# Performance work log

Hardware: AMD Instinct MI355X
Metric: run time of the kernel (lower is better)

The kernel has to match this reference:

```python
import jax, jax.numpy as jnp
import numpy as np
from math import sqrt

EPS = 1e-5
N_BISECT = 30

def _entmax15_impl(x):
    # alpha=1.5 entmax along last axis via bisection (entmax_bisect, alpha=1.5)
    xs = x * 0.5  # (alpha-1) * x
    mx = jnp.max(xs, axis=-1, keepdims=True)
    d = xs.shape[-1]
    lo = mx - 1.0
    hi = mx - d ** -0.5  # d^{-(alpha-1)}
    def body(i, carry):
        lo, hi = carry
        mid = 0.5 * (lo + hi)
        f = jnp.sum(jnp.square(jnp.maximum(xs - mid, 0.0)), -1, keepdims=True) - 1.0
        lo = jnp.where(f > 0, mid, lo)
        hi = jnp.where(f > 0, hi, mid)
        return lo, hi
    lo, hi = jax.lax.fori_loop(0, N_BISECT, body, (lo, hi))
    tau = 0.5 * (lo + hi)
    p = jnp.square(jnp.maximum(xs - tau, 0.0))
    return p / jnp.sum(p, -1, keepdims=True)

@jax.custom_vjp
def entmax15(x):
    return _entmax15_impl(x)

def _entmax15_fwd(x):
    p = _entmax15_impl(x)
    return p, p

def _entmax15_bwd(p, g):
    # exact entmax-1.5 backward (entmax repo): gppr = sqrt(p) on support
    s = jnp.sqrt(p)
    dx = g * s
    q = jnp.sum(dx, -1, keepdims=True) / jnp.sum(s, -1, keepdims=True)
    return (dx - q * s,)

entmax15.defvjp(_entmax15_fwd, _entmax15_bwd)

def layer_norm(x, g, b):
    m = jnp.mean(x, -1, keepdims=True)
    v = jnp.var(x, -1, keepdims=True)
    return (x - m) / jnp.sqrt(v + EPS) * g + b

def mlp(x, w1, b1, w2, b2):
    return jax.nn.gelu(x @ w1 + b1, approximate=False) @ w2 + b2

def hopfield_core(q_in, k_in, H, wq, bq, wk, bk, wv, bv, wo, bo):
    # Faithful to Hopfield.forward with mix=True; `values` arg of the torch
    # module is ignored (it recomputes value_projection(key_projection(keys))).
    B, L, _ = q_in.shape
    S = k_in.shape[1]
    q = (q_in @ wq + bq).reshape(B, L, H, -1)
    k = k_in @ wk + bk
    v = (k @ wv + bv).reshape(B, S, H, -1)
    kh = k.reshape(B, S, H, -1)
    E = q.shape[-1]
    scores = jnp.einsum('blhe,bshe->bhls', q, kh) * (1.0 / sqrt(E))
    A = entmax15(scores)
    out = jnp.einsum('bhls,bshd->blhd', A, v)
    # mix=True: transpose(2,1) then view(B, L, -1) on contiguous (B,H,L,D)
    out = jnp.transpose(out, (0, 2, 1, 3)).reshape(B, L, -1)
    return out @ wo + bo

def _forward(n_heads, x, ct_wq, ct_bq, ct_wk, ct_bk, ct_wv, ct_bv, ct_wo, ct_bo,
             cs_wq, cs_bq, cs_wk, cs_bk, cs_wv, cs_bv, cs_wo, cs_bo, cs_key,
             hp_wq, hp_bq, hp_wk, hp_bk, hp_wv, hp_bv, hp_wo, hp_bo,
             n1_g, n1_b, n2_g, n2_b, n3_g, n3_b, n4_g, n4_b,
             m1_w1, m1_b1, m1_w2, m1_b2, m2_w1, m2_b1, m2_w2, m2_b2):
    b, ts_d, seg, d = x.shape
    time_in = x.reshape(b * ts_d, seg, d)
    time_enc = hopfield_core(time_in, time_in, n_heads,
                             ct_wq, ct_bq, ct_wk, ct_bk, ct_wv, ct_bv, ct_wo, ct_bo)
    dim_in = layer_norm(time_in + time_enc, n1_g, n1_b)
    dim_in = layer_norm(dim_in + mlp(dim_in, m1_w1, m1_b1, m1_w2, m1_b2), n2_g, n2_b)
    # '(b ts_d) seg d -> (b seg) ts_d d'
    series_in = dim_in.reshape(b, ts_d, seg, d).transpose(0, 2, 1, 3).reshape(b * seg, ts_d, d)
    # HopfieldPooling: learned stored patterns as keys
    pooled_keys = jnp.broadcast_to(cs_key, (b * seg,) + cs_key.shape[1:])
    series_h = hopfield_core(series_in, pooled_keys, n_heads,
                             cs_wq, cs_bq, cs_wk, cs_bk, cs_wv, cs_bv, cs_wo, cs_bo)
    pooled_h = hopfield_core(series_in, series_in, n_heads,
                             hp_wq, hp_bq, hp_wk, hp_bk, hp_wv, hp_bv, hp_wo, hp_bo)
    dim_enc = layer_norm(series_h + pooled_h, n3_g, n3_b)
    dim_enc = layer_norm(dim_enc + mlp(dim_enc, m2_w1, m2_b1, m2_w2, m2_b2), n4_g, n4_b)
    # '(b seg) ts_d d -> b ts_d seg d'
    return dim_enc.reshape(b, seg, ts_d, d).transpose(0, 2, 1, 3)

def setup_inputs() -> dict:
    b, ts_d, seg, d, h, dff, factor = 8, 32, 64, 1024, 16, 4096, 10
    keys = iter(jax.random.split(jax.random.key(0), 64))
    def rn(shape, s=0.02):
        return jax.random.normal(next(keys), shape, jnp.float32) * s
    inp = {"x": jax.random.normal(next(keys), (b, ts_d, seg, d), jnp.float32)}
    for p in ("ct", "cs", "hp"):
        inp[p + "_wq"] = rn((d, d)); inp[p + "_bq"] = rn((d,))
        inp[p + "_wk"] = rn((d, d)); inp[p + "_bk"] = rn((d,))
        inp[p + "_wv"] = rn((d, d)); inp[p + "_bv"] = rn((d,))
        inp[p + "_wo"] = rn((d, d)); inp[p + "_bo"] = rn((d,))
    inp["cs_key"] = rn((1, factor, d), 0.1)
    for i in ("1", "2", "3", "4"):
        inp["n" + i + "_g"] = jnp.ones((d,), jnp.float32)
        inp["n" + i + "_b"] = jnp.zeros((d,), jnp.float32)
    for m in ("m1", "m2"):
        inp[m + "_w1"] = rn((d, dff)); inp[m + "_b1"] = rn((dff,))
        inp[m + "_w2"] = rn((dff, d)); inp[m + "_b2"] = rn((d,))
    inp["n_heads"] = h
    return inp

def reference(x, ct_wq, ct_bq, ct_wk, ct_bk, ct_wv, ct_bv, ct_wo, ct_bo,
              cs_wq, cs_bq, cs_wk, cs_bk, cs_wv, cs_bv, cs_wo, cs_bo, cs_key,
              hp_wq, hp_bq, hp_wk, hp_bk, hp_wv, hp_bv, hp_wo, hp_bo,
              n1_g, n1_b, n2_g, n2_b, n3_g, n3_b, n4_g, n4_b,
              m1_w1, m1_b1, m1_w2, m1_b2, m2_w1, m2_b1, m2_w2, m2_b2, n_heads):
    return _forward(n_heads, x, ct_wq, ct_bq, ct_wk, ct_bk, ct_wv, ct_bv, ct_wo, ct_bo,
                    cs_wq, cs_bq, cs_wk, cs_bk, cs_wv, cs_bv, cs_wo, cs_bo, cs_key,
                    hp_wq, hp_bq, hp_wk, hp_bk, hp_wv, hp_bv, hp_wo, hp_bo,
                    n1_g, n1_b, n2_g, n2_b, n3_g, n3_b, n4_g, n4_b,
                    m1_w1, m1_b1, m1_w2, m1_b2, m2_w1, m2_b1, m2_w2, m2_b2)
```

## Files before the change

### kernel.cpp

```cpp
#include <hip/hip_runtime.h>
#include <cstdio>

typedef __bf16 bf16x8 __attribute__((ext_vector_type(8)));
typedef float f32x4 __attribute__((ext_vector_type(4)));
typedef int i32x4 __attribute__((ext_vector_type(4)));
typedef unsigned short u16x4 __attribute__((ext_vector_type(4)));

__device__ __forceinline__ float bf2f(unsigned short u) {
  union { unsigned int i; float f; } x; x.i = ((unsigned int)u) << 16; return x.f;
}
__device__ __forceinline__ unsigned short f2bf(float f) {
  union { float f; unsigned int i; } x; x.f = f;
  unsigned int r = x.i + 0x7fffu + ((x.i >> 16) & 1u);
  return (unsigned short)(r >> 16);
}

__device__ __forceinline__ void gl2lds16(const unsigned short* g, unsigned short* l) {
  __builtin_amdgcn_global_load_lds((const __attribute__((address_space(1))) unsigned int*)g,
                                   (__attribute__((address_space(3))) unsigned int*)l, 16, 0, 0);
}

__global__ __launch_bounds__(256) void k_cast(const float* __restrict__ in,
                                              unsigned short* __restrict__ out, int n4) {
  int i = blockIdx.x * 256 + threadIdx.x;
  if (i >= n4) return;
  f32x4 v = ((const f32x4*)in)[i];
  u16x4 o;
  o[0] = f2bf(v[0]); o[1] = f2bf(v[1]); o[2] = f2bf(v[2]); o[3] = f2bf(v[3]);
  ((u16x4*)out)[i] = o;
}

__global__ __launch_bounds__(256) void k_tcast(const float* __restrict__ src,
                                               unsigned short* __restrict__ dst,
                                               int K, int N) {
  __shared__ float tile[32][33];
  int gx = blockIdx.x * 32;
  int gy = blockIdx.y * 32;
  int t = threadIdx.x;
  int c = t & 31, r0 = t >> 5;
#pragma unroll
  for (int i = 0; i < 4; i++) {
    int r = r0 + i * 8;
    tile[r][c] = src[(size_t)(gy + r) * N + gx + c];
  }
  __syncthreads();
#pragma unroll
  for (int i = 0; i < 4; i++) {
    int r = r0 + i * 8;
    dst[(size_t)(gx + r) * K + gy + c] = f2bf(tile[c][r]);
  }
}

__global__ __launch_bounds__(256) void k_bfold(const float* __restrict__ bk,
                                               const float* __restrict__ wv,
                                               const float* __restrict__ bv,
                                               float* __restrict__ out) {
  int n = blockIdx.x * 256 + threadIdx.x;
  float acc = bv[n];
#pragma unroll 8
  for (int j = 0; j < 1024; j++) acc += bk[j] * wv[(size_t)j * 1024 + n];
  out[n] = acc;
}

__global__ __launch_bounds__(256) void k_cpb(const float* __restrict__ a,
                                             const float* __restrict__ b,
                                             float* __restrict__ out) {
  int t = blockIdx.x * 256 + threadIdx.x;
  out[t] = a[t];
  out[1024 + t] = b[t];
}

template <bool GELU>
__global__ __launch_bounds__(256) void k_gemm(const unsigned short* __restrict__ A,
                                              const unsigned short* __restrict__ Bt,
                                              const float* __restrict__ bias,
                                              unsigned short* __restrict__ C,
                                              int M, int N, int K) {
  __shared__ unsigned short As[3][128 * 32];
  __shared__ unsigned short Bs[3][128 * 32];
  const int rowA0 = blockIdx.y * 128, colB0 = blockIdx.x * 128;
  const int t = threadIdx.x, w = t >> 6, lane = t & 63;
  const int wr = w >> 1, wc = w & 1;
  const int srow = w * 16 + (lane >> 2);
  const int schunk = (lane & 3) ^ ((lane >> 3) & 3);
  const unsigned short* pa = A + (size_t)(rowA0 + srow) * K + schunk * 8;
  const unsigned short* pb = Bt + (size_t)(colB0 + srow) * K + schunk * 8;
  const size_t row64 = (size_t)64 * K;

  f32x4 acc[4][4] = {};
  const int g = lane >> 4, ra = lane & 15;
  const int gp8 = (g ^ ((ra >> 1) & 3)) * 8;

  auto stage = [&](int buf, int kk) {
    gl2lds16(pa + kk,         &As[buf][w * 512]);
    gl2lds16(pa + row64 + kk, &As[buf][2048 + w * 512]);
    gl2lds16(pb + kk,         &Bs[buf][w * 512]);
    gl2lds16(pb + row64 + kk, &Bs[buf][2048 + w * 512]);
  };

  const int NT = K >> 5;
  stage(0, 0);
  if (NT > 1) stage(1, 32);
  int cur = 0;
  for (int j = 0; j < NT; ++j) {
    if (j + 1 < NT) asm volatile("s_waitcnt vmcnt(4)" ::: "memory");
    else            asm volatile("s_waitcnt vmcnt(0)" ::: "memory");
    __builtin_amdgcn_sched_barrier(0);
    __builtin_amdgcn_s_barrier();
    __builtin_amdgcn_sched_barrier(0);
    if (j + 2 < NT) {
      int nb = cur + 2; if (nb >= 3) nb -= 3;
      stage(nb, (j + 2) * 32);
    }
    bf16x8 af[4], bfr[4];
#pragma unroll
    for (int m = 0; m < 4; m++)
      af[m] = *(const bf16x8*)&As[cur][(wr * 64 + m * 16 + ra) * 32 + gp8];
#pragma unroll
    for (int n = 0; n < 4; n++)
      bfr[n] = *(const bf16x8*)&Bs[cur][(wc * 64 + n * 16 + ra) * 32 + gp8];
#pragma unroll
    for (int m = 0; m < 4; m++)
#pragma unroll
      for (int n = 0; n < 4; n++)
        acc[m][n] = __builtin_amdgcn_mfma_f32_16x16x32_bf16(af[m], bfr[n], acc[m][n], 0, 0, 0);
    cur += 1; if (cur >= 3) cur -= 3;
  }
  asm volatile("s_waitcnt vmcnt(0) lgkmcnt(0)" ::: "memory");
  __builtin_amdgcn_s_barrier();

  unsigned short* Ep = &As[0][0] + w * 1024;
  const int grow0 = rowA0 + wr * 64;
  const int gcol0 = colB0 + wc * 64;
  float bv[4];
#pragma unroll
  for (int n = 0; n < 4; n++) bv[n] = bias ? bias[gcol0 + n * 16 + ra] : 0.f;
  const int rdrow = lane >> 3, rg = lane & 7;
#pragma unroll
  for (int m = 0; m < 4; m++) {
#pragma unroll
    for (int n = 0; n < 4; n++)
#pragma unroll
      for (int i = 0; i < 4; i++) {
        int r = g * 4 + i;
        float v = acc[m][n][i] + bv[n];
        if (GELU) v = 0.5f * v * (1.f + erff(v * 0.70710678118654752f));
        Ep[r * 64 + ((ra + n * 16) ^ ((r & 7) << 3))] = f2bf(v);
      }
    asm volatile("s_waitcnt lgkmcnt(0)" ::: "memory");
    __builtin_amdgcn_sched_barrier(0);
#pragma unroll
    for (int p = 0; p < 2; p++) {
      int rr = p * 8 + rdrow;
      bf16x8 val = *(const bf16x8*)&Ep[rr * 64 + ((rg ^ (rr & 7)) << 3)];
      *(bf16x8*)&C[(size_t)(grow0 + m * 16 + rr) * N + gcol0 + rg * 8] = val;
    }
    asm volatile("s_waitcnt lgkmcnt(0)" ::: "memory");
  }
}

__global__ __launch_bounds__(256) void k_gemm10(const unsigned short* __restrict__ A,
                                                const unsigned short* __restrict__ Bt,
                                                const float* __restrict__ bias,
                                                unsigned short* __restrict__ C) {
  __shared__ float af[1024];
  int m = blockIdx.x, nb = blockIdx.y;
  int t = threadIdx.x;
#pragma unroll
  for (int i = 0; i < 4; i++) af[t * 4 + i] = bf2f(A[(size_t)m * 1024 + t * 4 + i]);
  __syncthreads();
  int w = t >> 6, lane = t & 63;
  for (int n = nb * 64 + w; n < nb * 64 + 64; n += 4) {
    const unsigned short* brow = Bt + (size_t)n * 1024 + lane * 16;
    float acc = 0.f;
#pragma unroll
    for (int j = 0; j < 16; j++) acc += af[lane * 16 + j] * bf2f(brow[j]);
#pragma unroll
    for (int o = 32; o; o >>= 1) acc += __shfl_xor(acc, o);
    if (lane == 0) C[(size_t)m * 1024 + n] = f2bf(acc + bias[n]);
  }
}

template <int L, int S, bool SHARED>
__global__ __launch_bounds__(256) void k_attn(const unsigned short* __restrict__ Q,
                                              const unsigned short* __restrict__ Kb,
                                              const unsigned short* __restrict__ Vb,
                                              unsigned short* __restrict__ Out, int RS) {
  constexpr int SP = (S <= 32) ? 32 : 64;
  constexpr int QST = 72;
  constexpr int VST = SP + 8;
  constexpr int CST = SP + 4;
  __shared__ unsigned short Qs[L * QST];
  __shared__ unsigned short Ks[SP * QST];
  __shared__ unsigned short Vt[64 * VST];
  __shared__ float Sc[L * CST];
  __shared__ float Rps[L];
  const int blk = blockIdx.x, batch = blk >> 4, h = blk & 15;
  const int t = threadIdx.x, w = t >> 6, lane = t & 63;

  for (int c = t; c < L * 8; c += 256) {
    int r = c >> 3, ch = (c & 7) * 8;
    *(i32x4*)&Qs[r * QST + ch] =
        *(const i32x4*)&Q[((size_t)(batch * L + r)) * RS + h * 64 + ch];
  }
  for (int c = t; c < SP * 8; c += 256) {
    int r = c >> 3, ch = (c & 7) * 8;
    i32x4 v = {0, 0, 0, 0};
    if (r < S) {
      size_t rb = SHARED ? (size_t)r : (size_t)(batch * S + r);
      v = *(const i32x4*)&Kb[rb * RS + h * 64 + ch];
    }
    *(i32x4*)&Ks[r * QST + ch] = v;
  }
  for (int c = t; c < SP * 64; c += 256) {
    int s = c >> 6, e = c & 63;
    unsigned short v = 0;
    if (s < S) {
      size_t rb = SHARED ? (size_t)s : (size_t)(batch * S + s);
      v = Vb[rb * RS + h * 64 + e];
    }
    Vt[e * VST + s] = v;
  }
  __syncthreads();

  const int ka = (lane >> 4) * 8, ra = lane & 15;
  const int cr = (lane >> 4) * 4, cc = lane & 15;
  constexpr int NT = SP / 16, TT = (L / 16) * NT;
  for (int tt = w; tt < TT; tt += 4) {
    int m = tt / NT, n = tt % NT;
    f32x4 a = {0.f, 0.f, 0.f, 0.f};
#pragma unroll
    for (int ks = 0; ks < 2; ks++) {
      bf16x8 af = *(const bf16x8*)&Qs[(m * 16 + ra) * QST + ks * 32 + ka];
      bf16x8 bf = *(const bf16x8*)&Ks[(n * 16 + ra) * QST + ks * 32 + ka];
      a = __builtin_amdgcn_mfma_f32_16x16x32_bf16(af, bf, a, 0, 0, 0);
    }
#pragma unroll
    for (int i = 0; i < 4; i++)
      Sc[(m * 16 + cr + i) * CST + n * 16 + cc] = a[i] * 0.0625f;
  }
  __syncthreads();

  constexpr int G = 256 / L, RW = 64 / G, SL = SP / G;
  const int row = w * RW + lane / G, sub = lane % G;
  float xs[SL];
#pragma unroll
  for (int j = 0; j < SL; j++) {
    int s = sub * SL + j;
    float v = Sc[row * CST + s];
    if (S < SP && s >= S) v = -1e30f;
    xs[j] = v;
  }
  float mx = xs[0];
#pragma unroll
  for (int j = 1; j < SL; j++) mx = fmaxf(mx, xs[j]);
#pragma unroll
  for (int o = G / 2; o; o >>= 1) mx = fmaxf(mx, __shfl_xor(mx, o));
  const float hoff = (S == 64) ? 0.125f : (S == 32) ? 0.17677669529663687f : 0.31622776601683794f;
  float lo = mx - 1.f, hi = mx - hoff;
#pragma unroll 1
  for (int it = 0; it < 26; it++) {
    float mid = 0.5f * (lo + hi);
    float f = 0.f;
#pragma unroll
    for (int j = 0; j < SL; j++) { float dd = fmaxf(xs[j] - mid, 0.f); f += dd * dd; }
#pragma unroll
    for (int o = G / 2; o; o >>= 1) f += __shfl_xor(f, o);
    bool gt = f > 1.f;
    lo = gt ? mid : lo;
    hi = gt ? hi : mid;
  }
  float tau = 0.5f * (lo + hi);
  float ps = 0.f;
#pragma unroll
  for (int j = 0; j < SL; j++) { float dd = fmaxf(xs[j] - tau, 0.f); xs[j] = dd * dd; ps += xs[j]; }
#pragma unroll
  for (int o = G / 2; o; o >>= 1) ps += __shfl_xor(ps, o);
  if (sub == 0) Rps[row] = 1.f / ps;
  unsigned short* Pb = Qs;
#pragma unroll
  for (int j = 0; j < SL; j += 4) {
    u16x4 pv;
#pragma unroll
    for (int jj = 0; jj < 4; jj++) pv[jj] = f2bf(xs[j + jj]);
    *(u16x4*)&Pb[row * VST + sub * SL + j] = pv;
  }
  __syncthreads();

  constexpr int TT2 = (L / 16) * 4;
  for (int tt = w; tt < TT2; tt += 4) {
    int m = tt >> 2, n = tt & 3;
    f32x4 a = {0.f, 0.f, 0.f, 0.f};
#pragma unroll
    for (int ks = 0; ks < SP / 32; ks++) {
      bf16x8 af = *(const bf16x8*)&Pb[(m * 16 + ra) * VST + ks * 32 + ka];
      bf16x8 bf = *(const bf16x8*)&Vt[(n * 16 + ra) * VST + ks * 32 + ka];
      a = __builtin_amdgcn_mfma_f32_16x16x32_bf16(af, bf, a, 0, 0, 0);
    }
#pragma unroll
    for (int i = 0; i < 4; i++) {
      int l = m * 16 + cr + i, e = n * 16 + cc;
      float val = a[i] * Rps[l];
      int l_new = h * (L / 16) + (l >> 4);
      int cg = (l & 15) * 64 + e;
      Out[((size_t)(batch * L + l_new)) * 1024 + cg] = f2bf(val);
    }
  }
}

template <int MODE, bool F32OUT>
__global__ __launch_bounds__(256) void k_ln(const unsigned short* __restrict__ a,
                                            const unsigned short* __restrict__ b,
                                            const float* __restrict__ g,
                                            const float* __restrict__ be,
                                            void* __restrict__ outp) {
  __shared__ float red[8];
  int r = blockIdx.x, t = threadIdx.x;
  size_t base = (size_t)r * 1024 + t * 4;
  u16x4 av = *(const u16x4*)(a + base);
  u16x4 bv = *(const u16x4*)(b + base);
  float x[4];
  float s = 0.f, ss = 0.f;
#pragma unroll
  for (int i = 0; i < 4; i++) {
    x[i] = bf2f(av[i]) + bf2f(bv[i]);
    s += x[i]; ss += x[i] * x[i];
  }
#pragma unroll
  for (int o = 32; o; o >>= 1) { s += __shfl_xor(s, o); ss += __shfl_xor(ss, o); }
  int w = t >> 6;
  if ((t & 63) == 0) { red[w] = s; red[4 + w] = ss; }
  __syncthreads();
  s = red[0] + red[1] + red[2] + red[3];
  ss = red[4] + red[5] + red[6] + red[7];
  float mean = s * (1.f / 1024.f);
  float var = ss * (1.f / 1024.f) - mean * mean;
  float rstd = rsqrtf(var + 1e-5f);
  int orow;
  if (MODE == 0) orow = r;
  else if (MODE == 1) { int bi = r >> 11, rem = r & 2047; int tt = rem >> 6, sd = rem & 63; orow = (bi << 11) + sd * 32 + tt; }
  else { int bi = r >> 11, rem = r & 2047; int sd = rem >> 5, tt = rem & 31; orow = (bi << 11) + tt * 64 + sd; }
  size_t ob = (size_t)orow * 1024 + t * 4;
  if (F32OUT) {
    f32x4 y;
#pragma unroll
    for (int i = 0; i < 4; i++) y[i] = (x[i] - mean) * rstd * g[t * 4 + i] + be[t * 4 + i];
    *(f32x4*)((float*)outp + ob) = y;
  } else {
    u16x4 y;
#pragma unroll
    for (int i = 0; i < 4; i++) y[i] = f2bf((x[i] - mean) * rstd * g[t * 4 + i] + be[t * 4 + i]);
    *(u16x4*)((unsigned short*)outp + ob) = y;
  }
}


extern "C" void kernel_launch(void* const* d_in, const int* in_sizes, int n_in,
                              void* d_out, int out_size, void* d_ws, size_t ws_size,
                              hipStream_t stream) {
  const int M = 16384;
  if (n_in < 43 || in_sizes[0] != 16777216 || in_sizes[25] != 10240 || in_sizes[34] != 4194304) {
    fprintf(stderr, "kernel_launch: unexpected input layout (n_in=%d)\n", n_in);
    return;
  }
  const float* x = (const float*)d_in[0];
  const float* w[3][4]; const float* bia[3][4];
  for (int p = 0; p < 3; p++) {
    w[p][0] = (const float*)d_in[1 + 8 * p + 0]; bia[p][0] = (const float*)d_in[1 + 8 * p + 1];
    w[p][1] = (const float*)d_in[1 + 8 * p + 2]; bia[p][1] = (const float*)d_in[1 + 8 * p + 3];
    w[p][2] = (const float*)d_in[1 + 8 * p + 4]; bia[p][2] = (const float*)d_in[1 + 8 * p + 5];
    w[p][3] = (const float*)d_in[1 + 8 * p + 6]; bia[p][3] = (const float*)d_in[1 + 8 * p + 7];
  }
  const float* cs_key = (const float*)d_in[25];
  const float* ng[4]; const float* nb[4];
  for (int i = 0; i < 4; i++) { ng[i] = (const float*)d_in[26 + 2 * i]; nb[i] = (const float*)d_in[27 + 2 * i]; }
  const float* m_w1[2]; const float* m_b1[2]; const float* m_w2[2]; const float* m_b2[2];
  for (int i = 0; i < 2; i++) {
    m_w1[i] = (const float*)d_in[34 + 4 * i]; m_b1[i] = (const float*)d_in[35 + 4 * i];
    m_w2[i] = (const float*)d_in[36 + 4 * i]; m_b2[i] = (const float*)d_in[37 + 4 * i];
  }

  char* base = (char*)d_ws; size_t off = 0;
  auto alloc = [&](size_t bytes) -> void* {
    off = (off + 255) & ~(size_t)255;
    void* p = base + off; off += bytes; return p;
  };
  const size_t W1M = (size_t)1024 * 1024;
  unsigned short* W3ct = (unsigned short*)alloc(3 * W1M * 2);
  unsigned short* W3hp = (unsigned short*)alloc(3 * W1M * 2);
  unsigned short* Woct = (unsigned short*)alloc(W1M * 2);
  unsigned short* Wohp = (unsigned short*)alloc(W1M * 2);
  unsigned short* Wocs = (unsigned short*)alloc(W1M * 2);
  unsigned short* Wqcs = (unsigned short*)alloc(W1M * 2);
  unsigned short* Wkcs = (unsigned short*)alloc(W1M * 2);
  unsigned short* Wvcs = (unsigned short*)alloc(W1M * 2);
  unsigned short* Wm1u = (unsigned short*)alloc((size_t)4096 * 1024 * 2);
  unsigned short* Wm1d = (unsigned short*)alloc((size_t)1024 * 4096 * 2);
  unsigned short* Wm2u = (unsigned short*)alloc((size_t)4096 * 1024 * 2);
  unsigned short* Wm2d = (unsigned short*)alloc((size_t)1024 * 4096 * 2);
  unsigned short* Wvt_ct = (unsigned short*)alloc(W1M * 2);
  unsigned short* Wraw_ct = (unsigned short*)alloc(W1M * 2);
  unsigned short* Wvt_hp = (unsigned short*)alloc(W1M * 2);
  unsigned short* Wraw_hp = (unsigned short*)alloc(W1M * 2);
  float* b3ct = (float*)alloc(3072 * 4);
  float* b3hp = (float*)alloc(3072 * 4);
  unsigned short* P[5];
  for (int i = 0; i < 5; i++) P[i] = (unsigned short*)alloc((size_t)M * 1024 * 2);
  unsigned short* KeyB = (unsigned short*)alloc((size_t)10 * 1024 * 2);
  unsigned short* Kcs = (unsigned short*)alloc((size_t)10 * 1024 * 2);
  unsigned short* Vcs = (unsigned short*)alloc((size_t)10 * 1024 * 2);
  if (off > ws_size) {
    fprintf(stderr, "kernel_launch: ws too small: need %zu have %zu\n", off, ws_size);
    return;
  }
  const int MC = 8192;

  auto gemm = [&](const unsigned short* Ap, const unsigned short* Bt, const float* bi,
                  unsigned short* Cp, int Mm, int Nn, int Kk, bool gelu) {
    dim3 gg(Nn / 128, Mm / 128);
    if (gelu) k_gemm<true><<<gg, 256, 0, stream>>>(Ap, Bt, bi, Cp, Mm, Nn, Kk);
    else      k_gemm<false><<<gg, 256, 0, stream>>>(Ap, Bt, bi, Cp, Mm, Nn, Kk);
  };
  auto tc = [&](const float* src, unsigned short* dst) {
    k_tcast<<<dim3(32, 32), 256, 0, stream>>>(src, dst, 1024, 1024);
  };

  tc(w[0][0], W3ct); tc(w[0][1], W3ct + W1M);
  tc(w[2][0], W3hp); tc(w[2][1], W3hp + W1M);
  tc(w[0][3], Woct); tc(w[2][3], Wohp); tc(w[1][3], Wocs);
  tc(w[1][0], Wqcs); tc(w[1][1], Wkcs); tc(w[1][2], Wvcs);
  k_tcast<<<dim3(128, 32), 256, 0, stream>>>(m_w1[0], Wm1u, 1024, 4096);
  k_tcast<<<dim3(32, 128), 256, 0, stream>>>(m_w2[0], Wm1d, 4096, 1024);
  k_tcast<<<dim3(128, 32), 256, 0, stream>>>(m_w1[1], Wm2u, 1024, 4096);
  k_tcast<<<dim3(32, 128), 256, 0, stream>>>(m_w2[1], Wm2d, 4096, 1024);
  tc(w[0][2], Wvt_ct); k_cast<<<1024, 256, 0, stream>>>(w[0][1], Wraw_ct, 262144);
  tc(w[2][2], Wvt_hp); k_cast<<<1024, 256, 0, stream>>>(w[2][1], Wraw_hp, 262144);
  k_cast<<<16384, 256, 0, stream>>>(x, P[0], 16777216 / 4);
  k_cast<<<10, 256, 0, stream>>>(cs_key, KeyB, 10240 / 4);
  gemm(Wvt_ct, Wraw_ct, nullptr, W3ct + 2 * W1M, 1024, 1024, 1024, false);
  gemm(Wvt_hp, Wraw_hp, nullptr, W3hp + 2 * W1M, 1024, 1024, 1024, false);
  k_cpb<<<4, 256, 0, stream>>>(bia[0][0], bia[0][1], b3ct);
  k_bfold<<<4, 256, 0, stream>>>(bia[0][1], w[0][2], bia[0][2], b3ct + 2048);
  k_cpb<<<4, 256, 0, stream>>>(bia[2][0], bia[2][1], b3hp);
  k_bfold<<<4, 256, 0, stream>>>(bia[2][1], w[2][2], bia[2][2], b3hp + 2048);
  k_gemm10<<<dim3(10, 16), 256, 0, stream>>>(KeyB, Wkcs, bia[1][1], Kcs);
  k_gemm10<<<dim3(10, 16), 256, 0, stream>>>(Kcs, Wvcs, bia[1][2], Vcs);

  gemm(P[0], W3ct, b3ct, P[1], M, 3072, 1024, false);
  k_attn<64, 64, false><<<256 * 16, 256, 0, stream>>>(P[1], P[1] + 1024, P[1] + 2048, P[4], 3072);
  gemm(P[4], Woct, bia[0][3], P[1], M, 1024, 1024, false);
  k_ln<0, false><<<M, 256, 0, stream>>>(P[0], P[1], ng[0], nb[0], P[2]);
  for (int c = 0; c < M; c += MC) {
    gemm(P[2] + (size_t)c * 1024, Wm1u, m_b1[0], P[3], MC, 4096, 1024, true);
    gemm(P[3], Wm1d, m_b2[0], P[1] + (size_t)c * 1024, MC, 1024, 4096, false);
  }
  k_ln<1, false><<<M, 256, 0, stream>>>(P[2], P[1], ng[1], nb[1], P[3]);

  gemm(P[3], W3hp, b3hp, P[0], M, 3072, 1024, false);
  k_attn<32, 32, false><<<512 * 16, 256, 0, stream>>>(P[0], P[0] + 1024, P[0] + 2048, P[4], 3072);
  gemm(P[4], Wohp, bia[2][3], P[1], M, 1024, 1024, false);
  gemm(P[3], Wqcs, bia[1][0], P[2], M, 1024, 1024, false);
  k_attn<32, 10, true><<<512 * 16, 256, 0, stream>>>(P[2], Kcs, Vcs, P[0], 1024);
  gemm(P[0], Wocs, bia[1][3], P[2], M, 1024, 1024, false);
  k_ln<0, false><<<M, 256, 0, stream>>>(P[2], P[1], ng[2], nb[2], P[0]);
  for (int c = 0; c < M; c += MC) {
    gemm(P[0] + (size_t)c * 1024, Wm2u, m_b1[1], P[2], MC, 4096, 1024, true);
    gemm(P[2], Wm2d, m_b2[1], P[1] + (size_t)c * 1024, MC, 1024, 4096, false);
  }
  k_ln<2, true><<<M, 256, 0, stream>>>(P[0], P[1], ng[3], nb[3], d_out);
}
```

Baseline: 1.825 ms.

## Switch main GEMMs to 256x256-tile 8-wave kernel with interleaved staging

```diff
diff --git a/kernel.cpp b/kernel.cpp
--- a/kernel.cpp
+++ b/kernel.cpp
@@ -71,11 +71,162 @@
 }
 
 template <bool GELU>
-__global__ __launch_bounds__(256) void k_gemm(const unsigned short* __restrict__ A,
-                                              const unsigned short* __restrict__ Bt,
-                                              const float* __restrict__ bias,
-                                              unsigned short* __restrict__ C,
-                                              int M, int N, int K) {
+__global__ __launch_bounds__(512, 2) void k_gemm8(const unsigned short* __restrict__ A,
+                                                  const unsigned short* __restrict__ Bt,
+                                                  const float* __restrict__ bias,
+                                                  unsigned short* __restrict__ C,
+                                                  int M, int N, int K) {
+  __shared__ unsigned short As[2][256 * 64];
+  __shared__ unsigned short Bs[2][256 * 64];
+  const int rowA0 = blockIdx.y * 256, colB0 = blockIdx.x * 256;
+  const int t = threadIdx.x, w = t >> 6, lane = t & 63;
+  const int wm = w >> 2, wn = w & 3;
+  const int g = lane >> 4, ra = lane & 15;
+  const int koff0 = (((0 * 4 + g) ^ (ra & 7)) * 8);
+  const int koff1 = (((1 * 4 + g) ^ (ra & 7)) * 8);
+  const int srow = w * 8 + (lane >> 3);
+  const int schunk = ((lane & 7) ^ ((lane >> 3) & 7)) * 8;
+
+  f32x4 acc[8][4] = {};
+
+  auto stageA = [&](int buf, int kk) {
+#pragma unroll
+    for (int gq = 0; gq < 4; gq++)
+      gl2lds16(A + (size_t)(rowA0 + gq * 64 + srow) * K + kk + schunk,
+               &As[buf][gq * 4096 + w * 512]);
+  };
+  auto stageB = [&](int buf, int kk) {
+#pragma unroll
+    for (int gq = 0; gq < 4; gq++)
+      gl2lds16(Bt + (size_t)(colB0 + gq * 64 + srow) * K + kk + schunk,
+               &Bs[buf][gq * 4096 + w * 512]);
+  };
+
+  const int NT = K >> 6;
+  stageA(0, 0); stageB(0, 0);
+  asm volatile("s_waitcnt vmcnt(0)" ::: "memory");
+  __builtin_amdgcn_sched_barrier(0);
+  __builtin_amdgcn_s_barrier();
+
+  bf16x8 aH[4][2], bH[2][2][2];
+  const int arow0 = wm * 128, brow0 = wn * 64;
+  for (int j = 0; j < NT; ++j) {
+    const int buf = j & 1;
+    const unsigned short* Ab = &As[buf][0];
+    const unsigned short* Bb = &Bs[buf][0];
+#pragma unroll
+    for (int fr = 0; fr < 4; fr++) {
+      aH[fr][0] = *(const bf16x8*)&Ab[(arow0 + fr * 16 + ra) * 64 + koff0];
+      aH[fr][1] = *(const bf16x8*)&Ab[(arow0 + fr * 16 + ra) * 64 + koff1];
+    }
+#pragma unroll
+    for (int fc = 0; fc < 2; fc++) {
+      bH[0][fc][0] = *(const bf16x8*)&Bb[(brow0 + fc * 16 + ra) * 64 + koff0];
+      bH[0][fc][1] = *(const bf16x8*)&Bb[(brow0 + fc * 16 + ra) * 64 + koff1];
+    }
+    if (j + 1 < NT) stageA(buf ^ 1, (j + 1) << 6);
+    __builtin_amdgcn_sched_barrier(0);
+    __builtin_amdgcn_s_barrier();
+    __builtin_amdgcn_sched_barrier(0);
+    __builtin_amdgcn_s_setprio(1);
+#pragma unroll
+    for (int fr = 0; fr < 4; fr++)
+#pragma unroll
+      for (int fc = 0; fc < 2; fc++)
+#pragma unroll
+        for (int ks = 0; ks < 2; ks++)
+          acc[fr][fc] = __builtin_amdgcn_mfma_f32_16x16x32_bf16(aH[fr][ks], bH[0][fc][ks], acc[fr][fc], 0, 0, 0);
+    __builtin_amdgcn_s_setprio(0);
+    __builtin_amdgcn_sched_barrier(0);
+    __builtin_amdgcn_s_barrier();
+#pragma unroll
+    for (int fc = 0; fc < 2; fc++) {
+      bH[1][fc][0] = *(const bf16x8*)&Bb[(brow0 + 32 + fc * 16 + ra) * 64 + koff0];
+      bH[1][fc][1] = *(const bf16x8*)&Bb[(brow0 + 32 + fc * 16 + ra) * 64 + koff1];
+    }
+    if (j + 1 < NT) stageB(buf ^ 1, (j + 1) << 6);
+    __builtin_amdgcn_sched_barrier(0);
+    __builtin_amdgcn_s_barrier();
+    __builtin_amdgcn_sched_barrier(0);
+    __builtin_amdgcn_s_setprio(1);
+#pragma unroll
+    for (int fr = 0; fr < 4; fr++)
+#pragma unroll
+      for (int fc = 0; fc < 2; fc++)
+#pragma unroll
+        for (int ks = 0; ks < 2; ks++)
+          acc[fr][2 + fc] = __builtin_amdgcn_mfma_f32_16x16x32_bf16(aH[fr][ks], bH[1][fc][ks], acc[fr][2 + fc], 0, 0, 0);
+    __builtin_amdgcn_s_setprio(0);
+    __builtin_amdgcn_sched_barrier(0);
+    __builtin_amdgcn_s_barrier();
+#pragma unroll
+    for (int fr = 0; fr < 4; fr++) {
+      aH[fr][0] = *(const bf16x8*)&Ab[(arow0 + 64 + fr * 16 + ra) * 64 + koff0];
+      aH[fr][1] = *(const bf16x8*)&Ab[(arow0 + 64 + fr * 16 + ra) * 64 + koff1];
+    }
+    __builtin_amdgcn_sched_barrier(0);
+    __builtin_amdgcn_s_barrier();
+    __builtin_amdgcn_sched_barrier(0);
+    __builtin_amdgcn_s_setprio(1);
+#pragma unroll
+    for (int fr = 0; fr < 4; fr++)
+#pragma unroll
+      for (int fc = 0; fc < 2; fc++)
+#pragma unroll
+        for (int ks = 0; ks < 2; ks++)
+          acc[4 + fr][fc] = __builtin_amdgcn_mfma_f32_16x16x32_bf16(aH[fr][ks], bH[0][fc][ks], acc[4 + fr][fc], 0, 0, 0);
+    __builtin_amdgcn_s_setprio(0);
+    __builtin_amdgcn_sched_barrier(0);
+    __builtin_amdgcn_s_barrier();
+    __builtin_amdgcn_s_setprio(1);
+#pragma unroll
+    for (int fr = 0; fr < 4; fr++)
+#pragma unroll
+      for (int fc = 0; fc < 2; fc++)
+#pragma unroll
+        for (int ks = 0; ks < 2; ks++)
+          acc[4 + fr][2 + fc] = __builtin_amdgcn_mfma_f32_16x16x32_bf16(aH[fr][ks], bH[1][fc][ks], acc[4 + fr][2 + fc], 0, 0, 0);
+    __builtin_amdgcn_s_setprio(0);
+    if (j + 1 < NT) asm volatile("s_waitcnt vmcnt(0)" ::: "memory");
+    __builtin_amdgcn_sched_barrier(0);
+    __builtin_amdgcn_s_barrier();
+  }
+
+  unsigned short* Ep = &As[0][0] + w * 1024;
+  const int grow0 = rowA0 + wm * 128;
+  const int gcol0 = colB0 + wn * 64;
+  float bv[4];
+#pragma unroll
+  for (int n = 0; n < 4; n++) bv[n] = bias ? bias[gcol0 + n * 16 + ra] : 0.f;
+  const int rdrow = lane >> 3, rg = lane & 7;
+#pragma unroll
+  for (int m = 0; m < 8; m++) {
+#pragma unroll
+    for (int n = 0; n < 4; n++)
+#pragma unroll
+      for (int i = 0; i < 4; i++) {
+        int r = g * 4 + i;
+        float v = acc[m][n][i] + bv[n];
+        if (GELU) v = 0.5f * v * (1.f + erff(v * 0.70710678118654752f));
+        Ep[r * 64 + ((ra + n * 16) ^ ((r & 7) << 3))] = f2bf(v);
+      }
+    asm volatile("s_waitcnt lgkmcnt(0)" ::: "memory");
+    __builtin_amdgcn_sched_barrier(0);
+#pragma unroll
+    for (int p = 0; p < 2; p++) {
+      int rr = p * 8 + rdrow;
+      bf16x8 val = *(const bf16x8*)&Ep[rr * 64 + ((rg ^ (rr & 7)) << 3)];
+      *(bf16x8*)&C[(size_t)(grow0 + m * 16 + rr) * N + gcol0 + rg * 8] = val;
+    }
+    asm volatile("s_waitcnt lgkmcnt(0)" ::: "memory");
+  }
+}
+
+__global__ __launch_bounds__(256) void k_gemmS(const unsigned short* __restrict__ A,
+                                               const unsigned short* __restrict__ Bt,
+                                               const float* __restrict__ bias,
+                                               unsigned short* __restrict__ C,
+                                               int M, int N, int K) {
   __shared__ unsigned short As[3][128 * 32];
   __shared__ unsigned short Bs[3][128 * 32];
   const int rowA0 = blockIdx.y * 128, colB0 = blockIdx.x * 128;
@@ -86,18 +237,15 @@
   const unsigned short* pa = A + (size_t)(rowA0 + srow) * K + schunk * 8;
   const unsigned short* pb = Bt + (size_t)(colB0 + srow) * K + schunk * 8;
   const size_t row64 = (size_t)64 * K;
-
   f32x4 acc[4][4] = {};
   const int g = lane >> 4, ra = lane & 15;
   const int gp8 = (g ^ ((ra >> 1) & 3)) * 8;
-
   auto stage = [&](int buf, int kk) {
-    gl2lds16(pa + kk,         &As[buf][w * 512]);
+    gl2lds16(pa + kk, &As[buf][w * 512]);
     gl2lds16(pa + row64 + kk, &As[buf][2048 + w * 512]);
-    gl2lds16(pb + kk,         &Bs[buf][w * 512]);
+    gl2lds16(pb + kk, &Bs[buf][w * 512]);
     gl2lds16(pb + row64 + kk, &Bs[buf][2048 + w * 512]);
   };
-
   const int NT = K >> 5;
   stage(0, 0);
   if (NT > 1) stage(1, 32);
@@ -105,13 +253,8 @@
   for (int j = 0; j < NT; ++j) {
     if (j + 1 < NT) asm volatile("s_waitcnt vmcnt(4)" ::: "memory");
     else            asm volatile("s_waitcnt vmcnt(0)" ::: "memory");
-    __builtin_amdgcn_sched_barrier(0);
-    __builtin_amdgcn_s_barrier();
-    __builtin_amdgcn_sched_barrier(0);
-    if (j + 2 < NT) {
-      int nb = cur + 2; if (nb >= 3) nb -= 3;
-      stage(nb, (j + 2) * 32);
-    }
+    __syncthreads();
+    if (j + 2 < NT) { int nb = cur + 2; if (nb >= 3) nb -= 3; stage(nb, (j + 2) * 32); }
     bf16x8 af[4], bfr[4];
 #pragma unroll
     for (int m = 0; m < 4; m++)
@@ -124,38 +267,21 @@
 #pragma unroll
       for (int n = 0; n < 4; n++)
         acc[m][n] = __builtin_amdgcn_mfma_f32_16x16x32_bf16(af[m], bfr[n], acc[m][n], 0, 0, 0);
+    __syncthreads();
     cur += 1; if (cur >= 3) cur -= 3;
   }
-  asm volatile("s_waitcnt vmcnt(0) lgkmcnt(0)" ::: "memory");
-  __builtin_amdgcn_s_barrier();
-
-  unsigned short* Ep = &As[0][0] + w * 1024;
-  const int grow0 = rowA0 + wr * 64;
-  const int gcol0 = colB0 + wc * 64;
-  float bv[4];
-#pragma unroll
-  for (int n = 0; n < 4; n++) bv[n] = bias ? bias[gcol0 + n * 16 + ra] : 0.f;
-  const int rdrow = lane >> 3, rg = lane & 7;
+  const int cr = g * 4, cc = ra;
 #pragma unroll
   for (int m = 0; m < 4; m++) {
-#pragma unroll
-    for (int n = 0; n < 4; n++)
-#pragma unroll
-      for (int i = 0; i < 4; i++) {
-        int r = g * 4 + i;
-        float v = acc[m][n][i] + bv[n];
-        if (GELU) v = 0.5f * v * (1.f + erff(v * 0.70710678118654752f));
-        Ep[r * 64 + ((ra + n * 16) ^ ((r & 7) << 3))] = f2bf(v);
-      }
-    asm volatile("s_waitcnt lgkmcnt(0)" ::: "memory");
-    __builtin_amdgcn_sched_barrier(0);
-#pragma unroll
-    for (int p = 0; p < 2; p++) {
-      int rr = p * 8 + rdrow;
-      bf16x8 val = *(const bf16x8*)&Ep[rr * 64 + ((rg ^ (rr & 7)) << 3)];
-      *(bf16x8*)&C[(size_t)(grow0 + m * 16 + rr) * N + gcol0 + rg * 8] = val;
-    }
-    asm volatile("s_waitcnt lgkmcnt(0)" ::: "memory");
+    int grow = rowA0 + wr * 64 + m * 16 + cr;
+#pragma unroll
+    for (int n = 0; n < 4; n++) {
+      int gcol = colB0 + wc * 64 + n * 16 + cc;
+      float bvv = bias ? bias[gcol] : 0.f;
+#pragma unroll
+      for (int i = 0; i < 4; i++)
+        C[(size_t)(grow + i) * N + gcol] = f2bf(acc[m][n][i] + bvv);
+    }
   }
 }
 
@@ -197,7 +323,6 @@
   __shared__ float Rps[L];
   const int blk = blockIdx.x, batch = blk >> 4, h = blk & 15;
   const int t = threadIdx.x, w = t >> 6, lane = t & 63;
-
   for (int c = t; c < L * 8; c += 256) {
     int r = c >> 3, ch = (c & 7) * 8;
     *(i32x4*)&Qs[r * QST + ch] =
@@ -222,7 +347,6 @@
     Vt[e * VST + s] = v;
   }
   __syncthreads();
-
   const int ka = (lane >> 4) * 8, ra = lane & 15;
   const int cr = (lane >> 4) * 4, cc = lane & 15;
   constexpr int NT = SP / 16, TT = (L / 16) * NT;
@@ -240,7 +364,6 @@
       Sc[(m * 16 + cr + i) * CST + n * 16 + cc] = a[i] * 0.0625f;
   }
   __syncthreads();
-
   constexpr int G = 256 / L, RW = 64 / G, SL = SP / G;
   const int row = w * RW + lane / G, sub = lane % G;
   float xs[SL];
@@ -286,7 +409,6 @@
     *(u16x4*)&Pb[row * VST + sub * SL + j] = pv;
   }
   __syncthreads();
-
   constexpr int TT2 = (L / 16) * 4;
   for (int tt = w; tt < TT2; tt += 4) {
     int m = tt >> 2, n = tt & 3;
@@ -398,28 +520,27 @@
   unsigned short* Wm1d = (unsigned short*)alloc((size_t)1024 * 4096 * 2);
   unsigned short* Wm2u = (unsigned short*)alloc((size_t)4096 * 1024 * 2);
   unsigned short* Wm2d = (unsigned short*)alloc((size_t)1024 * 4096 * 2);
-  unsigned short* Wvt_ct = (unsigned short*)alloc(W1M * 2);
-  unsigned short* Wraw_ct = (unsigned short*)alloc(W1M * 2);
-  unsigned short* Wvt_hp = (unsigned short*)alloc(W1M * 2);
-  unsigned short* Wraw_hp = (unsigned short*)alloc(W1M * 2);
   float* b3ct = (float*)alloc(3072 * 4);
   float* b3hp = (float*)alloc(3072 * 4);
-  unsigned short* P[5];
-  for (int i = 0; i < 5; i++) P[i] = (unsigned short*)alloc((size_t)M * 1024 * 2);
   unsigned short* KeyB = (unsigned short*)alloc((size_t)10 * 1024 * 2);
   unsigned short* Kcs = (unsigned short*)alloc((size_t)10 * 1024 * 2);
   unsigned short* Vcs = (unsigned short*)alloc((size_t)10 * 1024 * 2);
+  unsigned short* S[6];
+  for (int i = 0; i < 6; i++) S[i] = (unsigned short*)alloc((size_t)M * 1024 * 2);
   if (off > ws_size) {
     fprintf(stderr, "kernel_launch: ws too small: need %zu have %zu\n", off, ws_size);
     return;
   }
-  const int MC = 8192;
+  unsigned short* Wvt_ct = S[1];
+  unsigned short* Wraw_ct = S[1] + W1M;
+  unsigned short* Wvt_hp = S[1] + 2 * W1M;
+  unsigned short* Wraw_hp = S[1] + 3 * W1M;
 
   auto gemm = [&](const unsigned short* Ap, const unsigned short* Bt, const float* bi,
                   unsigned short* Cp, int Mm, int Nn, int Kk, bool gelu) {
-    dim3 gg(Nn / 128, Mm / 128);
-    if (gelu) k_gemm<true><<<gg, 256, 0, stream>>>(Ap, Bt, bi, Cp, Mm, Nn, Kk);
-    else      k_gemm<false><<<gg, 256, 0, stream>>>(Ap, Bt, bi, Cp, Mm, Nn, Kk);
+    dim3 gg(Nn / 256, Mm / 256);
+    if (gelu) k_gemm8<true><<<gg, 512, 0, stream>>>(Ap, Bt, bi, Cp, Mm, Nn, Kk);
+    else      k_gemm8<false><<<gg, 512, 0, stream>>>(Ap, Bt, bi, Cp, Mm, Nn, Kk);
   };
   auto tc = [&](const float* src, unsigned short* dst) {
     k_tcast<<<dim3(32, 32), 256, 0, stream>>>(src, dst, 1024, 1024);
@@ -435,10 +556,10 @@
   k_tcast<<<dim3(32, 128), 256, 0, stream>>>(m_w2[1], Wm2d, 4096, 1024);
   tc(w[0][2], Wvt_ct); k_cast<<<1024, 256, 0, stream>>>(w[0][1], Wraw_ct, 262144);
   tc(w[2][2], Wvt_hp); k_cast<<<1024, 256, 0, stream>>>(w[2][1], Wraw_hp, 262144);
-  k_cast<<<16384, 256, 0, stream>>>(x, P[0], 16777216 / 4);
+  k_cast<<<16384, 256, 0, stream>>>(x, S[0], 16777216 / 4);
   k_cast<<<10, 256, 0, stream>>>(cs_key, KeyB, 10240 / 4);
-  gemm(Wvt_ct, Wraw_ct, nullptr, W3ct + 2 * W1M, 1024, 1024, 1024, false);
-  gemm(Wvt_hp, Wraw_hp, nullptr, W3hp + 2 * W1M, 1024, 1024, 1024, false);
+  k_gemmS<<<dim3(8, 8), 256, 0, stream>>>(Wvt_ct, Wraw_ct, nullptr, W3ct + 2 * W1M, 1024, 1024, 1024);
+  k_gemmS<<<dim3(8, 8), 256, 0, stream>>>(Wvt_hp, Wraw_hp, nullptr, W3hp + 2 * W1M, 1024, 1024, 1024);
   k_cpb<<<4, 256, 0, stream>>>(bia[0][0], bia[0][1], b3ct);
   k_bfold<<<4, 256, 0, stream>>>(bia[0][1], w[0][2], bia[0][2], b3ct + 2048);
   k_cpb<<<4, 256, 0, stream>>>(bia[2][0], bia[2][1], b3hp);
@@ -446,26 +567,22 @@
   k_gemm10<<<dim3(10, 16), 256, 0, stream>>>(KeyB, Wkcs, bia[1][1], Kcs);
   k_gemm10<<<dim3(10, 16), 256, 0, stream>>>(Kcs, Wvcs, bia[1][2], Vcs);
 
-  gemm(P[0], W3ct, b3ct, P[1], M, 3072, 1024, false);
-  k_attn<64, 64, false><<<256 * 16, 256, 0, stream>>>(P[1], P[1] + 1024, P[1] + 2048, P[4], 3072);
-  gemm(P[4], Woct, bia[0][3], P[1], M, 1024, 1024, false);
-  k_ln<0, false><<<M, 256, 0, stream>>>(P[0], P[1], ng[0], nb[0], P[2]);
-  for (int c = 0; c < M; c += MC) {
-    gemm(P[2] + (size_t)c * 1024, Wm1u, m_b1[0], P[3], MC, 4096, 1024, true);
-    gemm(P[3], Wm1d, m_b2[0], P[1] + (size_t)c * 1024, MC, 1024, 4096, false);
-  }
-  k_ln<1, false><<<M, 256, 0, stream>>>(P[2], P[1], ng[1], nb[1], P[3]);
-
-  gemm(P[3], W3hp, b3hp, P[0], M, 3072, 1024, false);
-  k_attn<32, 32, false><<<512 * 16, 256, 0, stream>>>(P[0], P[0] + 1024, P[0] + 2048, P[4], 3072);
-  gemm(P[4], Wohp, bia[2][3], P[1], M, 1024, 1024, false);
-  gemm(P[3], Wqcs, bia[1][0], P[2], M, 1024, 1024, false);
-  k_attn<32, 10, true><<<512 * 16, 256, 0, stream>>>(P[2], Kcs, Vcs, P[0], 1024);
-  gemm(P[0], Wocs, bia[1][3], P[2], M, 1024, 1024, false);
-  k_ln<0, false><<<M, 256, 0, stream>>>(P[2], P[1], ng[2], nb[2], P[0]);
-  for (int c = 0; c < M; c += MC) {
-    gemm(P[0] + (size_t)c * 1024, Wm2u, m_b1[1], P[2], MC, 4096, 1024, true);
-    gemm(P[2], Wm2d, m_b2[1], P[1] + (size_t)c * 1024, MC, 1024, 4096, false);
-  }
-  k_ln<2, true><<<M, 256, 0, stream>>>(P[0], P[1], ng[3], nb[3], d_out);
-}
+  gemm(S[0], W3ct, b3ct, S[1], M, 3072, 1024, false);
+  k_attn<64, 64, false><<<256 * 16, 256, 0, stream>>>(S[1], S[1] + 1024, S[1] + 2048, S[4], 3072);
+  gemm(S[4], Woct, bia[0][3], S[5], M, 1024, 1024, false);
+  k_ln<0, false><<<M, 256, 0, stream>>>(S[0], S[5], ng[0], nb[0], S[1]);
+  gemm(S[1], Wm1u, m_b1[0], S[2], M, 4096, 1024, true);
+  gemm(S[2], Wm1d, m_b2[0], S[0], M, 1024, 4096, false);
+  k_ln<1, false><<<M, 256, 0, stream>>>(S[1], S[0], ng[1], nb[1], S[2]);
+
+  gemm(S[2], W3hp, b3hp, S[3], M, 3072, 1024, false);
+  k_attn<32, 32, false><<<512 * 16, 256, 0, stream>>>(S[3], S[3] + 1024, S[3] + 2048, S[0], 3072);
+  gemm(S[0], Wohp, bia[2][3], S[1], M, 1024, 1024, false);
+  gemm(S[2], Wqcs, bia[1][0], S[3], M, 1024, 1024, false);
+  k_attn<32, 10, true><<<512 * 16, 256, 0, stream>>>(S[3], Kcs, Vcs, S[4], 1024);
+  gemm(S[4], Wocs, bia[1][3], S[5], M, 1024, 1024, false);
+  k_ln<0, false><<<M, 256, 0, stream>>>(S[5], S[1], ng[2], nb[2], S[0]);
+  gemm(S[0], Wm2u, m_b1[1], S[1], M, 4096, 1024, true);
+  gemm(S[1], Wm2d, m_b2[1], S[5], M, 1024, 4096, false);
+  k_ln<2, true><<<M, 256, 0, stream>>>(S[0], S[5], ng[3], nb[3], d_out);
+}
```

After: 1.671 ms. 8.4% less time.
